# Kernel tuning notes

Measured on AMD Instinct MI355X. Metric: run time of the kernel, lower is better.

Reference implementation:

```python
import jax, jax.numpy as jnp
import numpy as np

B, S, DM, H, DK, DH = 8, 1024, 512, 8, 32, 64
LN_EPS = 1e-5
NEG_SLOPE = 0.01  # torch LeakyReLU default


def _l2norm(t, axis=-1, eps=1e-12):
    # matches F.normalize(p=2): x / max(||x||, eps)
    n = jnp.sqrt(jnp.sum(t * t, axis=axis, keepdims=True))
    return t / jnp.maximum(n, eps)


def _layernorm(t, w, b, eps=LN_EPS):
    mu = jnp.mean(t, axis=-1, keepdims=True)
    var = jnp.mean((t - mu) ** 2, axis=-1, keepdims=True)
    return (t - mu) * jax.lax.rsqrt(var + eps) * w + b


def setup_inputs() -> dict:
    key = jax.random.key(0)
    ks = jax.random.split(key, 16)
    x = jax.random.normal(ks[0], (B, S, DM), dtype=jnp.float32)
    # causal-style mask: True = masked (upper triangle)
    attn_mask = jnp.broadcast_to(jnp.triu(jnp.ones((S, S), dtype=bool), k=1), (B, S, S))
    pairwise_dist = jax.random.uniform(ks[1], (B, S, S), dtype=jnp.float32)
    s = 0.02
    return {
        "x": x,
        "attn_mask": attn_mask,
        "pairwise_dist": pairwise_dist,
        "Wq": jax.random.normal(ks[2], (H, DK, DM), dtype=jnp.float32) * s,
        "Wk": jax.random.normal(ks[3], (H, DK, DM), dtype=jnp.float32) * s,
        "Wv": jax.random.normal(ks[4], (H, DH, DM), dtype=jnp.float32) * s,
        "omega": jnp.ones((H,), dtype=jnp.float32),
        "Wo": jax.random.normal(ks[5], (DM, H * DH), dtype=jnp.float32) * s,
        "bo": jnp.zeros((DM,), dtype=jnp.float32),
        "Wf": jax.random.normal(ks[6], (DM, DM), dtype=jnp.float32) * s,
        "bf": jnp.zeros((DM,), dtype=jnp.float32),
        "ln1_w": jnp.ones((DM,), dtype=jnp.float32),
        "ln1_b": jnp.zeros((DM,), dtype=jnp.float32),
        "ln2_w": jnp.ones((DM,), dtype=jnp.float32),
        "ln2_b": jnp.zeros((DM,), dtype=jnp.float32),
    }


def _encoder_layer(x, attn_mask, pairwise_dist, Wq, Wk, Wv, omega,
                   Wo, bo, Wf, bf, ln1_w, ln1_b, ln2_w, ln2_b):
    # --- multi-head self-attention, all heads batched ---
    q = _l2norm(jnp.einsum('bsd,hkd->hbsk', x, Wq))   # [H,B,S,DK]
    k = _l2norm(jnp.einsum('bsd,hkd->hbsk', x, Wk))
    v = jnp.einsum('bsd,hvd->hbsv', x, Wv)            # [H,B,S,DH]
    scores = jnp.einsum('hbsk,hbtk->hbst', q, k)      # cosine-sim, [H,B,S,S]
    # distance bias: exp(-omega*d) - 1, detached in the original
    r = jax.lax.stop_gradient(
        jnp.exp(-omega[:, None, None, None] * pairwise_dist[None]) - 1.0)
    scores = scores + r
    scores = jnp.where(attn_mask[None], -jnp.inf, scores)
    # custom softmax: exp(x) / (sum + 1); exp(-inf)=0 handles masking
    z = jnp.exp(scores)
    attn = z / (jnp.sum(z, axis=-1, keepdims=True) + 1.0)
    y = jnp.einsum('hbst,hbtv->hbsv', attn, v)        # [H,B,S,DH]
    y = jnp.transpose(y, (1, 2, 0, 3)).reshape(x.shape[0], x.shape[1], -1)  # concat heads
    x_attn = y @ Wo.T + bo
    # --- residual + LN + FFN (dropout p=0 -> identity) ---
    z1 = _layernorm(x + x_attn, ln1_w, ln1_b)
    z_ff = jax.nn.leaky_relu(z1 @ Wf.T + bf, negative_slope=NEG_SLOPE)
    return _layernorm(z1 + z_ff, ln2_w, ln2_b)


def reference(x, attn_mask, pairwise_dist, Wq, Wk, Wv, omega,
              Wo, bo, Wf, bf, ln1_w, ln1_b, ln2_w, ln2_b):
    return _encoder_layer(x, attn_mask, pairwise_dist, Wq, Wk, Wv, omega,
                          Wo, bo, Wf, bf, ln1_w, ln1_b, ln2_w, ln2_b)
```

## Files before the change

kernel.cpp:

```cpp
#include <hip/hip_runtime.h>
#include <hip/hip_bf16.h>
#include <math.h>
#include <stdint.h>

#define BB 8
#define SS 1024
#define DMM 512
#define HH 8
#define DKK 32
#define DHH 64

typedef __bf16 bf16x8 __attribute__((ext_vector_type(8)));
typedef float f32x4 __attribute__((ext_vector_type(4)));

__device__ __forceinline__ void gll16(const void* g, void* l) {
  __builtin_amdgcn_global_load_lds(
      (const __attribute__((address_space(1))) void*)(uintptr_t)g,
      (__attribute__((address_space(3))) void*)(uint32_t)(uintptr_t)l,
      16, 0, 0);
}

__device__ __forceinline__ uint4 pack8(const float4 a, const float4 b) {
  union { __hip_bfloat162 h2[4]; uint4 u; } p;
  p.h2[0] = __float22bfloat162_rn(make_float2(a.x, a.y));
  p.h2[1] = __float22bfloat162_rn(make_float2(a.z, a.w));
  p.h2[2] = __float22bfloat162_rn(make_float2(b.x, b.y));
  p.h2[3] = __float22bfloat162_rn(make_float2(b.z, b.w));
  return p.u;
}

__global__ __launch_bounds__(256) void cvt_f32_bf16(
    const float* __restrict__ s, __bf16* __restrict__ d) {
  size_t i = ((size_t)blockIdx.x * 256 + threadIdx.x) * 8;
  float4 a = *(const float4*)&s[i];
  float4 b = *(const float4*)&s[i + 4];
  *(uint4*)&d[i] = pack8(a, b);
}

__global__ __launch_bounds__(256) void cvt_wqkv(
    const float* __restrict__ Wq, const float* __restrict__ Wk,
    const float* __restrict__ Wv, __bf16* __restrict__ d) {
  size_t i = ((size_t)blockIdx.x * 256 + threadIdx.x) * 8;
  const float* s;
  size_t off;
  if (i < 131072) { s = Wq; off = i; }
  else if (i < 262144) { s = Wk; off = i - 131072; }
  else { s = Wv; off = i - 262144; }
  float4 a = *(const float4*)&s[off];
  float4 b = *(const float4*)&s[off + 4];
  *(uint4*)&d[i] = pack8(a, b);
}

__global__ __launch_bounds__(256) void cvt_wof(
    const float* __restrict__ Wo, const float* __restrict__ Wf,
    __bf16* __restrict__ dWo, __bf16* __restrict__ dWf) {
  size_t i = ((size_t)blockIdx.x * 256 + threadIdx.x) * 8;
  const float* s;
  __bf16* d;
  size_t off;
  if (i < 262144) { s = Wo; d = dWo; off = i; }
  else { s = Wf; d = dWf; off = i - 262144; }
  float4 a = *(const float4*)&s[off];
  float4 b = *(const float4*)&s[off + 4];
  *(uint4*)&d[off] = pack8(a, b);
}

template <int MODE>
__global__ __launch_bounds__(256) void gemm_bf16(
    const __bf16* __restrict__ A, const __bf16* __restrict__ W,
    const float* __restrict__ bias, const float* __restrict__ resid,
    float* __restrict__ C, int N) {
  __shared__ __bf16 As[128 * 32];
  __shared__ __bf16 Bs[128 * 32];
  const int tid = threadIdx.x;
  const int n0 = blockIdx.x * 128;
  const int m0 = blockIdx.y * 128;
  const int lane = tid & 63;
  const int w = tid >> 6;
  const int wm = (w & 1) * 64, wn = (w >> 1) * 64;
  const int fr = lane & 15, quad = lane >> 4;

  const int srow = lane >> 2;
  const int schunk = (lane & 3) ^ ((lane >> 3) & 3);

  f32x4 acc[4][4];
#pragma unroll
  for (int mi = 0; mi < 4; ++mi)
#pragma unroll
    for (int ni = 0; ni < 4; ++ni) acc[mi][ni] = (f32x4){0.f, 0.f, 0.f, 0.f};

  for (int kt = 0; kt < 512; kt += 32) {
    __syncthreads();
#pragma unroll
    for (int j = 0; j < 2; ++j) {
      const int seg = w * 2 + j;
      const int row = seg * 16 + srow;
      gll16(&A[(size_t)(m0 + row) * 512 + kt + schunk * 8], &As[seg * 512]);
      gll16(&W[(size_t)(n0 + row) * 512 + kt + schunk * 8], &Bs[seg * 512]);
    }
    __syncthreads();

    bf16x8 af[4], bf[4];
    const int rsw = (quad ^ ((fr >> 1) & 3)) * 8;
#pragma unroll
    for (int mi = 0; mi < 4; ++mi)
      af[mi] = *(const bf16x8*)&As[(wm + mi * 16 + fr) * 32 + rsw];
#pragma unroll
    for (int ni = 0; ni < 4; ++ni)
      bf[ni] = *(const bf16x8*)&Bs[(wn + ni * 16 + fr) * 32 + rsw];
#pragma unroll
    for (int mi = 0; mi < 4; ++mi)
#pragma unroll
      for (int ni = 0; ni < 4; ++ni)
        acc[mi][ni] = __builtin_amdgcn_mfma_f32_16x16x32_bf16(
            af[mi], bf[ni], acc[mi][ni], 0, 0, 0);
  }

  const int er = (lane >> 4) * 4;
  const int ec = lane & 15;
#pragma unroll
  for (int mi = 0; mi < 4; ++mi) {
#pragma unroll
    for (int ni = 0; ni < 4; ++ni) {
      const int n = n0 + wn + ni * 16 + ec;
      float bsv = (MODE != 0) ? bias[n] : 0.0f;
#pragma unroll
      for (int r = 0; r < 4; ++r) {
        const int m = m0 + wm + mi * 16 + er + r;
        float v = acc[mi][ni][r];
        if (MODE == 1) {
          v += bsv + resid[(size_t)m * 512 + n];
        } else if (MODE == 2) {
          float g = v + bsv;
          g = g > 0.f ? g : 0.01f * g;
          v = resid[(size_t)m * 512 + n] + g;
        }
        C[(size_t)m * N + n] = v;
      }
    }
  }
}

__global__ __launch_bounds__(256) void prep_qkv(
    const float* __restrict__ qkv, __bf16* __restrict__ Qg,
    __bf16* __restrict__ Kg, __bf16* __restrict__ Vt) {
  __shared__ __bf16 vt[64][136];
  const int bh = blockIdx.x;
  const int b = bh >> 3, h = bh & 7;
  const int sb = blockIdx.y * 128;
  const int tid = threadIdx.x;

  {
    const int row = tid >> 1, half = tid & 1;
    const size_t rb = ((size_t)b * 1024 + sb + row) * 1024;
    {
      const float* p = qkv + rb + h * 32 + half * 16;
      float4 a[4];
      float ss = 0.f;
#pragma unroll
      for (int i = 0; i < 4; ++i) {
        a[i] = ((const float4*)p)[i];
        ss += a[i].x * a[i].x + a[i].y * a[i].y + a[i].z * a[i].z + a[i].w * a[i].w;
      }
      ss += __shfl_xor(ss, 1, 64);
      float sc = 1.0f / fmaxf(sqrtf(ss), 1e-12f);
      float4 s0 = make_float4(a[0].x * sc, a[0].y * sc, a[0].z * sc, a[0].w * sc);
      float4 s1 = make_float4(a[1].x * sc, a[1].y * sc, a[1].z * sc, a[1].w * sc);
      float4 s2 = make_float4(a[2].x * sc, a[2].y * sc, a[2].z * sc, a[2].w * sc);
      float4 s3 = make_float4(a[3].x * sc, a[3].y * sc, a[3].z * sc, a[3].w * sc);
      uint4* o = (uint4*)(Qg + ((size_t)bh * 1024 + sb + row) * 32 + half * 16);
      o[0] = pack8(s0, s1);
      o[1] = pack8(s2, s3);
    }
    {
      const float* p = qkv + rb + 256 + h * 32 + half * 16;
      float4 a[4];
      float ss = 0.f;
#pragma unroll
      for (int i = 0; i < 4; ++i) {
        a[i] = ((const float4*)p)[i];
        ss += a[i].x * a[i].x + a[i].y * a[i].y + a[i].z * a[i].z + a[i].w * a[i].w;
      }
      ss += __shfl_xor(ss, 1, 64);
      float sc = 1.0f / fmaxf(sqrtf(ss), 1e-12f);
      float4 s0 = make_float4(a[0].x * sc, a[0].y * sc, a[0].z * sc, a[0].w * sc);
      float4 s1 = make_float4(a[1].x * sc, a[1].y * sc, a[1].z * sc, a[1].w * sc);
      float4 s2 = make_float4(a[2].x * sc, a[2].y * sc, a[2].z * sc, a[2].w * sc);
      float4 s3 = make_float4(a[3].x * sc, a[3].y * sc, a[3].z * sc, a[3].w * sc);
      uint4* o = (uint4*)(Kg + ((size_t)bh * 1024 + sb + row) * 32 + half * 16);
      o[0] = pack8(s0, s1);
      o[1] = pack8(s2, s3);
    }
  }

#pragma unroll
  for (int i = 0; i < 8; ++i) {
    int idx = tid + i * 256;
    int t = idx >> 4, vd4 = (idx & 15) * 4;
    float4 v = *(const float4*)&qkv[((size_t)b * 1024 + sb + t) * 1024 + 512 + h * 64 + vd4];
    vt[vd4 + 0][t] = (__bf16)v.x;
    vt[vd4 + 1][t] = (__bf16)v.y;
    vt[vd4 + 2][t] = (__bf16)v.z;
    vt[vd4 + 3][t] = (__bf16)v.w;
  }
  __syncthreads();
  {
    const int vd = tid >> 2, tseg = (tid & 3) * 32;
    uint4* o = (uint4*)(Vt + (size_t)bh * 65536 + (size_t)vd * 1024 + sb + tseg);
#pragma unroll
    for (int j = 0; j < 4; ++j)
      o[j] = *(const uint4*)&vt[vd][tseg + j * 8];
  }
}

__global__ __launch_bounds__(256) void attn_mfma(
    const __bf16* __restrict__ Qg, const __bf16* __restrict__ Kg,
    const __bf16* __restrict__ Vt, const float* __restrict__ dist,
    const float* __restrict__ omega, __bf16* __restrict__ y) {
  __shared__ __bf16 Qs[64 * 32];
  __shared__ __bf16 Ks[64 * 32];
  __shared__ __bf16 Vs[64 * 64];
  __shared__ __bf16 zs[64][72];

  const int b = blockIdx.x;
  const int s0 = (15 - blockIdx.y) * 64;
  const int h = blockIdx.z;
  const int bh = b * 8 + h;
  const int tid = threadIdx.x;
  const int lane = tid & 63;
  const int w = tid >> 6;
  const int quad = lane >> 4;
  const int m = lane & 15;
  const float om = omega[h];
  const size_t rowbase = (size_t)b * SS;

  {
    int row = tid >> 2, p = tid & 3;
    uint4 v = *(const uint4*)(Qg + ((size_t)bh * 1024 + s0 + row) * 32 + p * 8);
    *(uint4*)&Qs[row * 32 + ((p ^ ((row >> 1) & 3)) * 8)] = v;
  }

  const int kswz = (quad ^ ((m >> 1) & 3)) * 8;
  const int sl = 16 * w + m;

  f32x4 acc[4];
#pragma unroll
  for (int ni = 0; ni < 4; ++ni) acc[ni] = (f32x4){0.f, 0.f, 0.f, 0.f};
  float zsum = 0.0f;
  const int ntiles = (s0 >> 6) + 1;

  for (int tt = 0; tt < ntiles; ++tt) {
    const int t0 = tt * 64;
    __syncthreads();
    {
      int row = tid >> 2, p = tid & 3;
      uint4 v = *(const uint4*)(Kg + ((size_t)bh * 1024 + t0 + row) * 32 + p * 8);
      *(uint4*)&Ks[row * 32 + ((p ^ ((row >> 1) & 3)) * 8)] = v;
    }
#pragma unroll
    for (int i = 0; i < 2; ++i) {
      int idx = tid + i * 256;
      int vd = idx >> 3, p = idx & 7;
      uint4 v = *(const uint4*)(Vt + (size_t)bh * 65536 + (size_t)vd * 1024 + t0 + p * 8);
      *(uint4*)&Vs[vd * 64 + ((p ^ (vd & 7)) * 8)] = v;
    }
    float4 dv[4];
#pragma unroll
    for (int mi = 0; mi < 4; ++mi)
      dv[mi] = *(const float4*)&dist[(rowbase + s0 + sl) * SS + t0 + 16 * mi + quad * 4];
    __syncthreads();

    const bf16x8 bq = *(const bf16x8*)&Qs[sl * 32 + kswz];
    f32x4 sc4[4];
#pragma unroll
    for (int mi = 0; mi < 4; ++mi) {
      const bf16x8 ak = *(const bf16x8*)&Ks[(16 * mi + m) * 32 + kswz];
      sc4[mi] = __builtin_amdgcn_mfma_f32_16x16x32_bf16(
          ak, bq, (f32x4){0.f, 0.f, 0.f, 0.f}, 0, 0, 0);
    }
    const bool diag = (tt == ntiles - 1);
#pragma unroll
    for (int mi = 0; mi < 4; ++mi) {
      float zr[4];
#pragma unroll
      for (int r = 0; r < 4; ++r) {
        float d = (&dv[mi].x)[r];
        float zv = __expf(sc4[mi][r] + __expf(-om * d) - 1.0f);
        if (diag && (16 * mi + quad * 4 + r) > sl) zv = 0.0f;
        zr[r] = zv;
        zsum += zv;
      }
      union { __hip_bfloat162 h2[2]; uint2 u; } pz;
      pz.h2[0] = __float22bfloat162_rn(make_float2(zr[0], zr[1]));
      pz.h2[1] = __float22bfloat162_rn(make_float2(zr[2], zr[3]));
      *(uint2*)&zs[sl][16 * mi + quad * 4] = pz.u;
    }
    __syncthreads();

    const bf16x8 za0 = *(const bf16x8*)&zs[sl][quad * 8];
    const bf16x8 za1 = *(const bf16x8*)&zs[sl][quad * 8 + 32];
#pragma unroll
    for (int ni = 0; ni < 4; ++ni) {
      const bf16x8 vb0 = *(const bf16x8*)&Vs[(16 * ni + m) * 64 + ((quad ^ (m & 7)) * 8)];
      const bf16x8 vb1 = *(const bf16x8*)&Vs[(16 * ni + m) * 64 + (((quad + 4) ^ (m & 7)) * 8)];
      acc[ni] = __builtin_amdgcn_mfma_f32_16x16x32_bf16(za0, vb0, acc[ni], 0, 0, 0);
      acc[ni] = __builtin_amdgcn_mfma_f32_16x16x32_bf16(za1, vb1, acc[ni], 0, 0, 0);
    }
  }

  zsum += __shfl_xor(zsum, 16, 64);
  zsum += __shfl_xor(zsum, 32, 64);

#pragma unroll
  for (int r = 0; r < 4; ++r) {
    float dn = __shfl(zsum, quad * 4 + r, 64);
    float inv = 1.0f / (dn + 1.0f);
    __bf16* yp = &y[(rowbase + s0 + 16 * w + quad * 4 + r) * 512 + h * 64 + m];
#pragma unroll
    for (int ni = 0; ni < 4; ++ni)
      yp[16 * ni] = (__bf16)(acc[ni][r] * inv);
  }
}

__global__ __launch_bounds__(256) void ln_kernel(
    const float* __restrict__ in, const float* __restrict__ w,
    const float* __restrict__ bvec, float* __restrict__ out,
    __bf16* __restrict__ outb) {
  __shared__ float sbuf[4];
  const int m = blockIdx.x;
  const int tid = threadIdx.x;
  const float2 v = ((const float2*)(in + (size_t)m * 512))[tid];
  float s = v.x + v.y;
#pragma unroll
  for (int off = 32; off > 0; off >>= 1) s += __shfl_down(s, off, 64);
  const int lane = tid & 63, wid = tid >> 6;
  if (lane == 0) sbuf[wid] = s;
  __syncthreads();
  const float mu = (sbuf[0] + sbuf[1] + sbuf[2] + sbuf[3]) * (1.0f / 512.0f);
  __syncthreads();
  const float dx = v.x - mu, dy = v.y - mu;
  float s2 = dx * dx + dy * dy;
#pragma unroll
  for (int off = 32; off > 0; off >>= 1) s2 += __shfl_down(s2, off, 64);
  if (lane == 0) sbuf[wid] = s2;
  __syncthreads();
  const float var = (sbuf[0] + sbuf[1] + sbuf[2] + sbuf[3]) * (1.0f / 512.0f);
  const float inv = rsqrtf(var + 1e-5f);
  const float2 wv = ((const float2*)w)[tid];
  const float2 bv = ((const float2*)bvec)[tid];
  float2 o;
  o.x = dx * inv * wv.x + bv.x;
  o.y = dy * inv * wv.y + bv.y;
  ((float2*)(out + (size_t)m * 512))[tid] = o;
  if (outb) {
    union { __hip_bfloat162 h2; unsigned u; } p;
    p.h2 = __float22bfloat162_rn(make_float2(o.x, o.y));
    *(unsigned*)&outb[(size_t)m * 512 + tid * 2] = p.u;
  }
}

extern "C" void kernel_launch(void* const* d_in, const int* in_sizes, int n_in,
                              void* d_out, int out_size, void* d_ws, size_t ws_size,
                              hipStream_t stream) {
  const float* x = (const float*)d_in[0];
  const float* dist = (const float*)d_in[2];
  const float* Wq = (const float*)d_in[3];
  const float* Wk = (const float*)d_in[4];
  const float* Wv = (const float*)d_in[5];
  const float* omega = (const float*)d_in[6];
  const float* Wo = (const float*)d_in[7];
  const float* bo = (const float*)d_in[8];
  const float* Wf = (const float*)d_in[9];
  const float* bf_ = (const float*)d_in[10];
  const float* ln1w = (const float*)d_in[11];
  const float* ln1b = (const float*)d_in[12];
  const float* ln2w = (const float*)d_in[13];
  const float* ln2b = (const float*)d_in[14];
  float* out = (float*)d_out;

  char* base = (char*)d_ws;
  const size_t MB = 1 << 20;
  float* qkv = (float*)base;
  __bf16* yb = (__bf16*)base;
  float* t1 = (float*)(base + 8 * MB);
  __bf16* t1b = (__bf16*)(base + 24 * MB);
  __bf16* xb = (__bf16*)(base + 32 * MB);
  __bf16* Wcat = (__bf16*)(base + 40 * MB);
  __bf16* Qg = (__bf16*)(base + 32 * MB);
  __bf16* Kg = (__bf16*)(base + 36 * MB);
  __bf16* Vt = (__bf16*)(base + 40 * MB);
  __bf16* Wob = (__bf16*)(base + 32 * MB);
  __bf16* Wfb = (__bf16*)(base + 32 * MB + 512 * 1024);

  dim3 blk(256);
  cvt_f32_bf16<<<dim3(2048), blk, 0, stream>>>(x, xb);
  cvt_wqkv<<<dim3(256), blk, 0, stream>>>(Wq, Wk, Wv, Wcat);
  gemm_bf16<0><<<dim3(8, 64), blk, 0, stream>>>(xb, Wcat, nullptr, nullptr,
                                                qkv, 1024);
  prep_qkv<<<dim3(64, 8), blk, 0, stream>>>(qkv, Qg, Kg, Vt);
  attn_mfma<<<dim3(8, 16, 8), blk, 0, stream>>>(Qg, Kg, Vt, dist, omega, yb);
  cvt_wof<<<dim3(256), blk, 0, stream>>>(Wo, Wf, Wob, Wfb);
  gemm_bf16<1><<<dim3(4, 64), blk, 0, stream>>>(yb, Wob, bo, x, t1, 512);
  ln_kernel<<<dim3(8192), blk, 0, stream>>>(t1, ln1w, ln1b, t1, t1b);
  gemm_bf16<2><<<dim3(4, 64), blk, 0, stream>>>(t1b, Wfb, bf_, t1, out, 512);
  ln_kernel<<<dim3(8192), blk, 0, stream>>>(out, ln2w, ln2b, out, nullptr);
}
```

Before: 263.7 us.

## Rewrite attention as single-wave blocks, merge input conversions, one-wave-per-row layernorm

Result: no change. 265.7 us (+0.7%).

```diff
diff --git a/kernel.cpp b/kernel.cpp
--- a/kernel.cpp
+++ b/kernel.cpp
@@ -29,26 +29,30 @@
   return p.u;
 }
 
-__global__ __launch_bounds__(256) void cvt_f32_bf16(
-    const float* __restrict__ s, __bf16* __restrict__ d) {
-  size_t i = ((size_t)blockIdx.x * 256 + threadIdx.x) * 8;
-  float4 a = *(const float4*)&s[i];
-  float4 b = *(const float4*)&s[i + 4];
-  *(uint4*)&d[i] = pack8(a, b);
-}
-
-__global__ __launch_bounds__(256) void cvt_wqkv(
-    const float* __restrict__ Wq, const float* __restrict__ Wk,
-    const float* __restrict__ Wv, __bf16* __restrict__ d) {
+__global__ __launch_bounds__(256) void cvt_pre(
+    const float* __restrict__ x, const float* __restrict__ Wq,
+    const float* __restrict__ Wk, const float* __restrict__ Wv,
+    __bf16* __restrict__ xb, __bf16* __restrict__ Wcat) {
   size_t i = ((size_t)blockIdx.x * 256 + threadIdx.x) * 8;
   const float* s;
+  __bf16* d;
   size_t off;
-  if (i < 131072) { s = Wq; off = i; }
-  else if (i < 262144) { s = Wk; off = i - 131072; }
-  else { s = Wv; off = i - 262144; }
+  if (i < 4194304) { s = x; d = xb; off = i; }
+  else {
+    size_t j = i - 4194304;
+    d = Wcat + j;
+    if (j < 131072) { s = Wq; off = j; }
+    else if (j < 262144) { s = Wk; off = j - 131072; }
+    else { s = Wv; off = j - 262144; }
+    d = Wcat + j - off + off;
+    float4 a = *(const float4*)&s[off];
+    float4 b = *(const float4*)&s[off + 4];
+    *(uint4*)&Wcat[j] = pack8(a, b);
+    return;
+  }
   float4 a = *(const float4*)&s[off];
   float4 b = *(const float4*)&s[off + 4];
-  *(uint4*)&d[i] = pack8(a, b);
+  *(uint4*)&d[off] = pack8(a, b);
 }
 
 __global__ __launch_bounds__(256) void cvt_wof(
@@ -213,112 +217,104 @@
   }
 }
 
-__global__ __launch_bounds__(256) void attn_mfma(
+__global__ __launch_bounds__(64, 4) void attn_wave(
     const __bf16* __restrict__ Qg, const __bf16* __restrict__ Kg,
     const __bf16* __restrict__ Vt, const float* __restrict__ dist,
     const float* __restrict__ omega, __bf16* __restrict__ y) {
-  __shared__ __bf16 Qs[64 * 32];
-  __shared__ __bf16 Ks[64 * 32];
-  __shared__ __bf16 Vs[64 * 64];
-  __shared__ __bf16 zs[64][72];
-
-  const int b = blockIdx.x;
-  const int s0 = (15 - blockIdx.y) * 64;
-  const int h = blockIdx.z;
-  const int bh = b * 8 + h;
-  const int tid = threadIdx.x;
-  const int lane = tid & 63;
-  const int w = tid >> 6;
-  const int quad = lane >> 4;
-  const int m = lane & 15;
+  __shared__ __bf16 zbuf[2][16][40];
+
+  const int idx = blockIdx.x;
+  const int sb2 = 31 - (idx >> 6);
+  const int bh = idx & 63;
+  const int b = bh >> 3, h = bh & 7;
+  const int lane = threadIdx.x & 63;
+  const int l15 = lane & 15;
+  const int q = lane >> 4;
   const float om = omega[h];
-  const size_t rowbase = (size_t)b * SS;
-
-  {
-    int row = tid >> 2, p = tid & 3;
-    uint4 v = *(const uint4*)(Qg + ((size_t)bh * 1024 + s0 + row) * 32 + p * 8);
-    *(uint4*)&Qs[row * 32 + ((p ^ ((row >> 1) & 3)) * 8)] = v;
-  }
-
-  const int kswz = (quad ^ ((m >> 1) & 3)) * 8;
-  const int sl = 16 * w + m;
-
-  f32x4 acc[4];
-#pragma unroll
-  for (int ni = 0; ni < 4; ++ni) acc[ni] = (f32x4){0.f, 0.f, 0.f, 0.f};
-  float zsum = 0.0f;
-  const int ntiles = (s0 >> 6) + 1;
-
-  for (int tt = 0; tt < ntiles; ++tt) {
-    const int t0 = tt * 64;
-    __syncthreads();
-    {
-      int row = tid >> 2, p = tid & 3;
-      uint4 v = *(const uint4*)(Kg + ((size_t)bh * 1024 + t0 + row) * 32 + p * 8);
-      *(uint4*)&Ks[row * 32 + ((p ^ ((row >> 1) & 3)) * 8)] = v;
-    }
-#pragma unroll
-    for (int i = 0; i < 2; ++i) {
-      int idx = tid + i * 256;
-      int vd = idx >> 3, p = idx & 7;
-      uint4 v = *(const uint4*)(Vt + (size_t)bh * 65536 + (size_t)vd * 1024 + t0 + p * 8);
-      *(uint4*)&Vs[vd * 64 + ((p ^ (vd & 7)) * 8)] = v;
-    }
-    float4 dv[4];
-#pragma unroll
-    for (int mi = 0; mi < 4; ++mi)
-      dv[mi] = *(const float4*)&dist[(rowbase + s0 + sl) * SS + t0 + 16 * mi + quad * 4];
-    __syncthreads();
-
-    const bf16x8 bq = *(const bf16x8*)&Qs[sl * 32 + kswz];
-    f32x4 sc4[4];
-#pragma unroll
-    for (int mi = 0; mi < 4; ++mi) {
-      const bf16x8 ak = *(const bf16x8*)&Ks[(16 * mi + m) * 32 + kswz];
-      sc4[mi] = __builtin_amdgcn_mfma_f32_16x16x32_bf16(
-          ak, bq, (f32x4){0.f, 0.f, 0.f, 0.f}, 0, 0, 0);
-    }
-    const bool diag = (tt == ntiles - 1);
-#pragma unroll
-    for (int mi = 0; mi < 4; ++mi) {
-      float zr[4];
+  const int s_base = sb2 * 32;
+
+  const __bf16* Qp = Qg + (size_t)bh * 32768;
+  const __bf16* Kp = Kg + (size_t)bh * 32768;
+  const __bf16* Vp = Vt + (size_t)bh * 65536;
+  const float* Dp = dist + ((size_t)b * 1024 + s_base) * 1024;
+
+  bf16x8 bq[2];
+#pragma unroll
+  for (int st = 0; st < 2; ++st)
+    bq[st] = *(const bf16x8*)&Qp[(size_t)(s_base + st * 16 + l15) * 32 + q * 8];
+
+  f32x4 acc[2][4];
+#pragma unroll
+  for (int st = 0; st < 2; ++st)
+#pragma unroll
+    for (int ni = 0; ni < 4; ++ni) acc[st][ni] = (f32x4){0.f, 0.f, 0.f, 0.f};
+  float zsum[2] = {0.f, 0.f};
+
+  const int nch = sb2 + 1;
+  for (int c = 0; c < nch; ++c) {
+    const int t0 = c * 32;
+    const bf16x8 ak0 = *(const bf16x8*)&Kp[(size_t)(t0 + l15) * 32 + q * 8];
+    const bf16x8 ak1 = *(const bf16x8*)&Kp[(size_t)(t0 + 16 + l15) * 32 + q * 8];
+    bf16x8 vb[4];
+#pragma unroll
+    for (int ni = 0; ni < 4; ++ni)
+      vb[ni] = *(const bf16x8*)&Vp[(size_t)(ni * 16 + l15) * 1024 + t0 + q * 8];
+
+#pragma unroll
+    for (int st = 0; st < 2; ++st) {
+      const int s = s_base + st * 16 + l15;
+      const float4 dv0 = *(const float4*)&Dp[(size_t)(st * 16 + l15) * 1024 + t0 + q * 4];
+      const float4 dv1 = *(const float4*)&Dp[(size_t)(st * 16 + l15) * 1024 + t0 + 16 + q * 4];
+      f32x4 s0 = __builtin_amdgcn_mfma_f32_16x16x32_bf16(
+          ak0, bq[st], (f32x4){0.f, 0.f, 0.f, 0.f}, 0, 0, 0);
+      f32x4 s1 = __builtin_amdgcn_mfma_f32_16x16x32_bf16(
+          ak1, bq[st], (f32x4){0.f, 0.f, 0.f, 0.f}, 0, 0, 0);
+      float z0[4], z1[4];
 #pragma unroll
       for (int r = 0; r < 4; ++r) {
-        float d = (&dv[mi].x)[r];
-        float zv = __expf(sc4[mi][r] + __expf(-om * d) - 1.0f);
-        if (diag && (16 * mi + quad * 4 + r) > sl) zv = 0.0f;
-        zr[r] = zv;
-        zsum += zv;
+        int t = t0 + q * 4 + r;
+        float zv = __expf(s0[r] + __expf(-om * (&dv0.x)[r]) - 1.0f);
+        z0[r] = (t <= s) ? zv : 0.0f;
+        t += 16;
+        zv = __expf(s1[r] + __expf(-om * (&dv1.x)[r]) - 1.0f);
+        z1[r] = (t <= s) ? zv : 0.0f;
+        zsum[st] += z0[r] + z1[r];
       }
-      union { __hip_bfloat162 h2[2]; uint2 u; } pz;
-      pz.h2[0] = __float22bfloat162_rn(make_float2(zr[0], zr[1]));
-      pz.h2[1] = __float22bfloat162_rn(make_float2(zr[2], zr[3]));
-      *(uint2*)&zs[sl][16 * mi + quad * 4] = pz.u;
-    }
-    __syncthreads();
-
-    const bf16x8 za0 = *(const bf16x8*)&zs[sl][quad * 8];
-    const bf16x8 za1 = *(const bf16x8*)&zs[sl][quad * 8 + 32];
-#pragma unroll
-    for (int ni = 0; ni < 4; ++ni) {
-      const bf16x8 vb0 = *(const bf16x8*)&Vs[(16 * ni + m) * 64 + ((quad ^ (m & 7)) * 8)];
-      const bf16x8 vb1 = *(const bf16x8*)&Vs[(16 * ni + m) * 64 + (((quad + 4) ^ (m & 7)) * 8)];
-      acc[ni] = __builtin_amdgcn_mfma_f32_16x16x32_bf16(za0, vb0, acc[ni], 0, 0, 0);
-      acc[ni] = __builtin_amdgcn_mfma_f32_16x16x32_bf16(za1, vb1, acc[ni], 0, 0, 0);
-    }
-  }
-
-  zsum += __shfl_xor(zsum, 16, 64);
-  zsum += __shfl_xor(zsum, 32, 64);
-
-#pragma unroll
-  for (int r = 0; r < 4; ++r) {
-    float dn = __shfl(zsum, quad * 4 + r, 64);
-    float inv = 1.0f / (dn + 1.0f);
-    __bf16* yp = &y[(rowbase + s0 + 16 * w + quad * 4 + r) * 512 + h * 64 + m];
-#pragma unroll
-    for (int ni = 0; ni < 4; ++ni)
-      yp[16 * ni] = (__bf16)(acc[ni][r] * inv);
+      union { __hip_bfloat162 h2[2]; uint2 u; } p0, p1;
+      p0.h2[0] = __float22bfloat162_rn(make_float2(z0[0], z0[1]));
+      p0.h2[1] = __float22bfloat162_rn(make_float2(z0[2], z0[3]));
+      p1.h2[0] = __float22bfloat162_rn(make_float2(z1[0], z1[1]));
+      p1.h2[1] = __float22bfloat162_rn(make_float2(z1[2], z1[3]));
+      *(uint2*)&zbuf[st][l15][q * 4] = p0.u;
+      *(uint2*)&zbuf[st][l15][16 + q * 4] = p1.u;
+    }
+#pragma unroll
+    for (int st = 0; st < 2; ++st) {
+      const bf16x8 az = *(const bf16x8*)&zbuf[st][l15][q * 8];
+#pragma unroll
+      for (int ni = 0; ni < 4; ++ni)
+        acc[st][ni] = __builtin_amdgcn_mfma_f32_16x16x32_bf16(
+            az, vb[ni], acc[st][ni], 0, 0, 0);
+    }
+  }
+
+#pragma unroll
+  for (int st = 0; st < 2; ++st) {
+    zsum[st] += __shfl_xor(zsum[st], 16, 64);
+    zsum[st] += __shfl_xor(zsum[st], 32, 64);
+  }
+
+#pragma unroll
+  for (int st = 0; st < 2; ++st) {
+#pragma unroll
+    for (int r = 0; r < 4; ++r) {
+      const float dn = __shfl(zsum[st], q * 4 + r, 64);
+      const float inv = 1.0f / (dn + 1.0f);
+      __bf16* yp = &y[((size_t)b * 1024 + s_base + st * 16 + q * 4 + r) * 512 + h * 64 + l15];
+#pragma unroll
+      for (int ni = 0; ni < 4; ++ni)
+        yp[ni * 16] = (__bf16)(acc[st][ni][r] * inv);
+    }
   }
 }
 
@@ -326,37 +322,31 @@
     const float* __restrict__ in, const float* __restrict__ w,
     const float* __restrict__ bvec, float* __restrict__ out,
     __bf16* __restrict__ outb) {
-  __shared__ float sbuf[4];
-  const int m = blockIdx.x;
-  const int tid = threadIdx.x;
-  const float2 v = ((const float2*)(in + (size_t)m * 512))[tid];
-  float s = v.x + v.y;
-#pragma unroll
-  for (int off = 32; off > 0; off >>= 1) s += __shfl_down(s, off, 64);
-  const int lane = tid & 63, wid = tid >> 6;
-  if (lane == 0) sbuf[wid] = s;
-  __syncthreads();
-  const float mu = (sbuf[0] + sbuf[1] + sbuf[2] + sbuf[3]) * (1.0f / 512.0f);
-  __syncthreads();
-  const float dx = v.x - mu, dy = v.y - mu;
-  float s2 = dx * dx + dy * dy;
-#pragma unroll
-  for (int off = 32; off > 0; off >>= 1) s2 += __shfl_down(s2, off, 64);
-  if (lane == 0) sbuf[wid] = s2;
-  __syncthreads();
-  const float var = (sbuf[0] + sbuf[1] + sbuf[2] + sbuf[3]) * (1.0f / 512.0f);
-  const float inv = rsqrtf(var + 1e-5f);
-  const float2 wv = ((const float2*)w)[tid];
-  const float2 bv = ((const float2*)bvec)[tid];
-  float2 o;
-  o.x = dx * inv * wv.x + bv.x;
-  o.y = dy * inv * wv.y + bv.y;
-  ((float2*)(out + (size_t)m * 512))[tid] = o;
-  if (outb) {
-    union { __hip_bfloat162 h2; unsigned u; } p;
-    p.h2 = __float22bfloat162_rn(make_float2(o.x, o.y));
-    *(unsigned*)&outb[(size_t)m * 512 + tid * 2] = p.u;
-  }
+  const int row = blockIdx.x * 4 + (threadIdx.x >> 6);
+  const int lane = threadIdx.x & 63;
+  const float4* ip = (const float4*)(in + (size_t)row * 512);
+  float4 a = ip[lane * 2], c = ip[lane * 2 + 1];
+  float s = a.x + a.y + a.z + a.w + c.x + c.y + c.z + c.w;
+#pragma unroll
+  for (int off = 32; off > 0; off >>= 1) s += __shfl_xor(s, off, 64);
+  const float mu = s * (1.0f / 512.0f);
+  a.x -= mu; a.y -= mu; a.z -= mu; a.w -= mu;
+  c.x -= mu; c.y -= mu; c.z -= mu; c.w -= mu;
+  float s2 = a.x * a.x + a.y * a.y + a.z * a.z + a.w * a.w +
+             c.x * c.x + c.y * c.y + c.z * c.z + c.w * c.w;
+#pragma unroll
+  for (int off = 32; off > 0; off >>= 1) s2 += __shfl_xor(s2, off, 64);
+  const float inv = rsqrtf(s2 * (1.0f / 512.0f) + 1e-5f);
+  const float4 w0 = ((const float4*)w)[lane * 2], w1 = ((const float4*)w)[lane * 2 + 1];
+  const float4 b0 = ((const float4*)bvec)[lane * 2], b1 = ((const float4*)bvec)[lane * 2 + 1];
+  float4 o0, o1;
+  o0.x = a.x * inv * w0.x + b0.x; o0.y = a.y * inv * w0.y + b0.y;
+  o0.z = a.z * inv * w0.z + b0.z; o0.w = a.w * inv * w0.w + b0.w;
+  o1.x = c.x * inv * w1.x + b1.x; o1.y = c.y * inv * w1.y + b1.y;
+  o1.z = c.z * inv * w1.z + b1.z; o1.w = c.w * inv * w1.w + b1.w;
+  float4* op = (float4*)(out + (size_t)row * 512);
+  op[lane * 2] = o0; op[lane * 2 + 1] = o1;
+  if (outb) *(uint4*)&outb[(size_t)row * 512 + lane * 8] = pack8(o0, o1);
 }
 
 extern "C" void kernel_launch(void* const* d_in, const int* in_sizes, int n_in,
@@ -393,15 +383,14 @@
   __bf16* Wfb = (__bf16*)(base + 32 * MB + 512 * 1024);
 
   dim3 blk(256);
-  cvt_f32_bf16<<<dim3(2048), blk, 0, stream>>>(x, xb);
-  cvt_wqkv<<<dim3(256), blk, 0, stream>>>(Wq, Wk, Wv, Wcat);
+  cvt_pre<<<dim3(2304), blk, 0, stream>>>(x, Wq, Wk, Wv, xb, Wcat);
   gemm_bf16<0><<<dim3(8, 64), blk, 0, stream>>>(xb, Wcat, nullptr, nullptr,
                                                 qkv, 1024);
   prep_qkv<<<dim3(64, 8), blk, 0, stream>>>(qkv, Qg, Kg, Vt);
-  attn_mfma<<<dim3(8, 16, 8), blk, 0, stream>>>(Qg, Kg, Vt, dist, omega, yb);
+  attn_wave<<<dim3(2048), dim3(64), 0, stream>>>(Qg, Kg, Vt, dist, omega, yb);
   cvt_wof<<<dim3(256), blk, 0, stream>>>(Wo, Wf, Wob, Wfb);
   gemm_bf16<1><<<dim3(4, 64), blk, 0, stream>>>(yb, Wob, bo, x, t1, 512);
-  ln_kernel<<<dim3(8192), blk, 0, stream>>>(t1, ln1w, ln1b, t1, t1b);
+  ln_kernel<<<dim3(2048), blk, 0, stream>>>(t1, ln1w, ln1b, t1, t1b);
   gemm_bf16<2><<<dim3(4, 64), blk, 0, stream>>>(t1b, Wfb, bf_, t1, out, 512);
-  ln_kernel<<<dim3(8192), blk, 0, stream>>>(out, ln2w, ln2b, out, nullptr);
-}
+  ln_kernel<<<dim3(2048), blk, 0, stream>>>(out, ln2w, ln2b, out, nullptr);
+}
```
